# Kernel tuning notes

Measured on AMD Instinct MI355X. Metric: run time of the kernel, lower is better.

Reference implementation:

```python
import jax, jax.numpy as jnp
import numpy as np

B, S, H, V = 32, 400, 512, 50000


def setup_inputs() -> dict:
    key = jax.random.key(0)
    ks = jax.random.split(key, 32)
    g = lambda i, shape: jax.random.normal(ks[i], shape, jnp.float32) * 0.05
    return {
        "x_id": jax.random.randint(ks[0], (B, S), 0, V, jnp.int32),
        "y_id": jax.random.randint(ks[1], (B, 1), 0, V, jnp.int32),
        "x_mask": jnp.zeros((B, S), jnp.int32),  # pad flag: 1 = pad
        "emb": g(2, (V, H)),
        "enc_fw_W": g(3, (H, 3 * H)), "enc_fw_U": g(4, (H, 3 * H)), "enc_fw_b": g(5, (2, 3 * H)),
        "enc_bw_W": g(6, (H, 3 * H)), "enc_bw_U": g(7, (H, 3 * H)), "enc_bw_b": g(8, (2, 3 * H)),
        "red_W": g(9, (2 * H, H)), "red_b": g(10, (H,)),
        "dec_W": g(11, (H, 3 * H)), "dec_U": g(12, (H, 3 * H)), "dec_b": g(13, (2, 3 * H)),
        "att_Wh": g(14, (2 * H, H)), "att_Ws": g(15, (H, H)), "att_bs": g(16, (H,)),
        "att_Wc": g(17, (1, 1)), "att_V": g(18, (H, 1)),
        "fc_W": g(19, (3 * H, H)), "fc_b": g(20, (H,)),
        "vocab_W": g(21, (H, V)),
        "pg_Wh": g(22, (2 * H, 1)), "pg_Ws": g(23, (H, 1)), "pg_Wx": g(24, (H, 1)), "pg_b": g(25, (1,)),
    }


def _gru_cell(h, xz, U, br):
    # Keras GRU, reset_after=True, gate order z, r, h
    hd = h.shape[-1]
    rec = h @ U + br
    z = jax.nn.sigmoid(xz[..., :hd] + rec[..., :hd])
    r = jax.nn.sigmoid(xz[..., hd:2 * hd] + rec[..., hd:2 * hd])
    hh = jnp.tanh(xz[..., 2 * hd:] + r * rec[..., 2 * hd:])
    return z * h + (1.0 - z) * hh


def _gru_scan(x, h0, W, U, b):
    xz = x @ W + b[0]  # [b,T,3H] -- input projections precomputed
    def step(h, xt):
        h = _gru_cell(h, xt, U, b[1])
        return h, h
    h_last, hs = jax.lax.scan(step, h0, jnp.swapaxes(xz, 0, 1))
    return jnp.swapaxes(hs, 0, 1), h_last


def reference(x_id, y_id, x_mask, emb, enc_fw_W, enc_fw_U, enc_fw_b, enc_bw_W, enc_bw_U, enc_bw_b,
              red_W, red_b, dec_W, dec_U, dec_b, att_Wh, att_Ws, att_bs, att_Wc, att_V,
              fc_W, fc_b, vocab_W, pg_Wh, pg_Ws, pg_Wx, pg_b):
    b, s = x_id.shape
    hid = enc_fw_U.shape[0]
    maskf = x_mask.astype(jnp.float32)
    # ---- encoder: single-layer BiGRU ----
    x_emb = emb[x_id]                                     # [b,S,H]
    h0 = jnp.zeros((b, hid), x_emb.dtype)
    fw_seq, fw_s = _gru_scan(x_emb, h0, enc_fw_W, enc_fw_U, enc_fw_b)
    bw_seq, bw_s = _gru_scan(x_emb[:, ::-1], h0, enc_bw_W, enc_bw_U, enc_bw_b)
    enc_seq = jnp.concatenate([fw_seq, bw_seq[:, ::-1]], -1)   # [b,S,2H]
    state = jax.nn.relu(jnp.concatenate([fw_s, bw_s], -1) @ red_W + red_b)  # [b,H]
    # ---- decoder: one GRU step ----
    y_emb = emb[y_id]                                     # [b,1,H]
    xz = y_emb[:, 0] @ dec_W + dec_b[0]
    dec_state = _gru_cell(state, xz, dec_U, dec_b[1])     # [b,H]
    dec_out = dec_state[:, None, :]                       # [b,1,H]
    # ---- Bahdanau attention with (zero-initialized) coverage ----
    e = enc_seq @ att_Wh + (dec_out @ att_Ws + att_bs)    # [b,S,H]
    cover = jnp.zeros((b, s, 1), e.dtype)
    e = e + cover @ att_Wc
    e = jnp.tanh(e) @ att_V                               # [b,S,1]
    e = e + maskf[..., None] * -1e10
    w = jax.nn.softmax(e, axis=-2)                        # [b,S,1]
    context = jnp.sum(w * enc_seq, axis=-2, keepdims=True)  # [b,1,2H]
    # ---- output projection + vocab softmax ----
    y_out = jnp.concatenate([dec_out, context], -1) @ fc_W + fc_b  # [b,1,H]
    vocab_dist = jax.nn.softmax(y_out[:, 0] @ vocab_W, axis=-1)    # [b,V]
    # ---- pointer gate ----
    p_gen = jax.nn.sigmoid(context[:, 0] @ pg_Wh + dec_state @ pg_Ws + y_emb[:, 0] @ pg_Wx + pg_b)  # [b,1]
    # ---- extended-vocab copy distribution (vectorized batched scatter-add) ----
    aw = w[..., 0] * (1.0 - maskf) * (1.0 - p_gen)        # [b,S]
    ext = jnp.pad(p_gen * vocab_dist, ((0, 0), (0, s)))   # [b,V+S]
    bidx = jnp.arange(b)[:, None]
    final = ext.at[bidx, x_id].add(aw)                    # [b,V+S]
    return final
```

## Files before the change

### kernel.cpp

```cpp
#include <hip/hip_runtime.h>
#include <math.h>

#define S_LEN 400
#define BATCH 32
#define HID   512
#define G3    1536
#define N2    3072
#define VOC   50000
#define OUTW  (VOC + S_LEN)

typedef unsigned long long ull;
typedef unsigned int uint;
typedef unsigned short ushort;
typedef short bf16x8 __attribute__((ext_vector_type(8)));
typedef float f32x4 __attribute__((ext_vector_type(4)));
typedef ushort u16x8 __attribute__((ext_vector_type(8)));

__device__ __forceinline__ float sigf(float x) { return 1.f / (1.f + __expf(-x)); }
__device__ __forceinline__ float tanh_fast(float x) {
  const float xc = fminf(fmaxf(x, -15.f), 15.f);
  const float e = __expf(-2.f * xc);
  return (1.f - e) / (1.f + e);
}
__device__ __forceinline__ ushort f2bf(float f) {
  uint u = __float_as_uint(f);
  u += 0x7FFFu + ((u >> 16) & 1u);
  return (ushort)(u >> 16);
}
__device__ __forceinline__ float bf2f(ushort h) {
  return __uint_as_float((uint)h << 16);
}
__device__ __forceinline__ float dot4(float4 a, float4 b) {
  return a.x*b.x + a.y*b.y + a.z*b.z + a.w*b.w;
}

__device__ void trans_tile_512(const float* __restrict__ srcA,
                               const float* __restrict__ srcB,
                               const int split, const int stride, const int Krows,
                               const int k0, const int n0,
                               ushort* __restrict__ dstH, float* __restrict__ dstF)
{
  __shared__ float tt[64][65];
  const int tid = threadIdx.x;
  const int j = tid & 63, i0 = tid >> 6;
  {
    const int n = n0 + j;
    const float* s = (n < split) ? (srcA + n) : (srcB + (n - split));
    #pragma unroll
    for (int i = i0; i < 64; i += 8)
      tt[i][j] = s[(size_t)(k0 + i) * stride];
  }
  __syncthreads();
  const int ii = tid & 63;
  if (dstH != nullptr) {
    #pragma unroll
    for (int jj = i0; jj < 64; jj += 8)
      dstH[(size_t)(n0 + jj) * Krows + k0 + ii] = f2bf(tt[ii][jj]);
  } else {
    #pragma unroll
    for (int jj = i0; jj < 64; jj += 8)
      dstF[(size_t)(n0 + jj) * Krows + k0 + ii] = tt[ii][jj];
  }
}

__global__ __launch_bounds__(512) void gru_scan(
    const ushort* __restrict__ xzm,
    const ushort* __restrict__ Utbf,
    const float* __restrict__ bfw, const float* __restrict__ bbw,
    float* __restrict__ enc_seq, ushort* __restrict__ enc_bf,
    ull* __restrict__ hpkt,
    const float* __restrict__ att_Wh, const float* __restrict__ red_W,
    const float* __restrict__ dec_W, const float* __restrict__ dec_U,
    const float* __restrict__ att_Ws, const float* __restrict__ fc_W,
    ushort* __restrict__ Whbf, float* __restrict__ redWt,
    float* __restrict__ decWUt, float* __restrict__ WsT,
    float* __restrict__ fcT)
{
  if (blockIdx.x >= 128) {
    const int tb = blockIdx.x - 128;
    if (tb < 128) {
      trans_tile_512(att_Wh, att_Wh, 512, 512, 1024,
                     (tb % 16) * 64, (tb / 16) * 64, Whbf, nullptr);
    } else if (tb < 256) {
      const int t = tb - 128;
      trans_tile_512(red_W, red_W, 512, 512, 1024,
                     (t % 16) * 64, (t / 16) * 64, nullptr, redWt);
    } else if (tb < 640) {
      const int t = tb - 256;
      trans_tile_512(dec_W, dec_U, G3, G3, 512,
                     (t % 8) * 64, (t / 8) * 64, nullptr, decWUt);
    } else if (tb < 704) {
      const int t = tb - 640;
      trans_tile_512(att_Ws, att_Ws, 512, 512, 512,
                     (t % 8) * 64, (t / 8) * 64, nullptr, WsT);
    } else {
      const int t = tb - 704;
      trans_tile_512(fc_W, fc_W, 512, 512, 1536,
                     (t % 24) * 64, (t / 24) * 64, nullptr, fcT);
    }
    return;
  }

  const int bid = blockIdx.x;
  const int group = bid & 7;
  const int dir = group >> 2;
  const int bg  = group & 3;
  const int ht  = bid >> 3;
  const int tid = threadIdx.x;
  const int lane = tid & 63;
  const int w  = tid >> 6;
  const int l15 = lane & 15;
  const int lk  = lane >> 4;

  const float* __restrict__ br = (dir ? bbw : bfw) + G3;

  const int gate = w % 3, jh = w / 3;
  bf16x8 ufrag[16];
  if (w < 6) {
    const ushort* ub = Utbf + ((size_t)dir * G3 + gate * 512 + ht * 32 + jh * 16 + l15) * 512
                     + lk * 8;
    #pragma unroll
    for (int s = 0; s < 16; ++s)
      ufrag[s] = *(const bf16x8*)(ub + s * 32);
  }

  __shared__ ushort h_bf[16][520];
  __shared__ float redm[3][8][32];

  for (int i = tid; i < 16 * 520; i += 512) ((ushort*)h_bf)[i] = 0;

  const int cb = w;
  const int gbi = tid >> 5;
  const int gj  = tid & 31;
  const int gjq = ht * 32 + gj;
  const int gb  = bg * 8 + (gbi & 7);
  const float brz = br[gjq], brr = br[512 + gjq], brh = br[1024 + gjq];

  ull* __restrict__ pk = hpkt + (size_t)dir * (2 * BATCH * HID);
  __syncthreads();

  for (int t = 0; t < S_LEN; ++t) {
    const int ts = dir ? (S_LEN - 1 - t) : t;

    float xzv0 = 0.f, xzv1 = 0.f, xzv2 = 0.f;
    if (tid < 256) {
      const ushort* xp = xzm + ((size_t)gb * S_LEN + ts) * N2 + dir * G3 + gjq;
      xzv0 = bf2f(xp[0]); xzv1 = bf2f(xp[512]); xzv2 = bf2f(xp[1024]);
    }

    float hold = 0.f;
    {
      ull* bp = pk + ((size_t)(t & 1) * BATCH + (bg * 8 + cb)) * HID + lane;
      ull* hp = pk + ((size_t)(t & 1) * BATCH + gb) * HID + gjq;
      const uint tu = (uint)t;
      for (;;) {
        ull v0 = __hip_atomic_load(bp,       __ATOMIC_RELAXED, __HIP_MEMORY_SCOPE_AGENT);
        ull v1 = __hip_atomic_load(bp + 64,  __ATOMIC_RELAXED, __HIP_MEMORY_SCOPE_AGENT);
        ull v2 = __hip_atomic_load(bp + 128, __ATOMIC_RELAXED, __HIP_MEMORY_SCOPE_AGENT);
        ull v3 = __hip_atomic_load(bp + 192, __ATOMIC_RELAXED, __HIP_MEMORY_SCOPE_AGENT);
        ull v4 = __hip_atomic_load(bp + 256, __ATOMIC_RELAXED, __HIP_MEMORY_SCOPE_AGENT);
        ull v5 = __hip_atomic_load(bp + 320, __ATOMIC_RELAXED, __HIP_MEMORY_SCOPE_AGENT);
        ull v6 = __hip_atomic_load(bp + 384, __ATOMIC_RELAXED, __HIP_MEMORY_SCOPE_AGENT);
        ull v7 = __hip_atomic_load(bp + 448, __ATOMIC_RELAXED, __HIP_MEMORY_SCOPE_AGENT);
        bool ok = ((uint)(v0 >> 32) == tu) & ((uint)(v1 >> 32) == tu)
                & ((uint)(v2 >> 32) == tu) & ((uint)(v3 >> 32) == tu)
                & ((uint)(v4 >> 32) == tu) & ((uint)(v5 >> 32) == tu)
                & ((uint)(v6 >> 32) == tu) & ((uint)(v7 >> 32) == tu);
        ull hv = 0;
        if (tid < 256) {
          hv = __hip_atomic_load(hp, __ATOMIC_RELAXED, __HIP_MEMORY_SCOPE_AGENT);
          ok &= ((uint)(hv >> 32) == tu);
        }
        if (__all(ok)) {
          h_bf[cb][lane]       = f2bf(__uint_as_float((uint)v0));
          h_bf[cb][lane + 64]  = f2bf(__uint_as_float((uint)v1));
          h_bf[cb][lane + 128] = f2bf(__uint_as_float((uint)v2));
          h_bf[cb][lane + 192] = f2bf(__uint_as_float((uint)v3));
          h_bf[cb][lane + 256] = f2bf(__uint_as_float((uint)v4));
          h_bf[cb][lane + 320] = f2bf(__uint_as_float((uint)v5));
          h_bf[cb][lane + 384] = f2bf(__uint_as_float((uint)v6));
          h_bf[cb][lane + 448] = f2bf(__uint_as_float((uint)v7));
          if (tid < 256) hold = __uint_as_float((uint)hv);
          break;
        }
        __builtin_amdgcn_s_sleep(1);
      }
    }
    __syncthreads();

    if (w < 6) {
      f32x4 acc = f32x4{0.f, 0.f, 0.f, 0.f};
      #pragma unroll
      for (int s = 0; s < 16; ++s) {
        const bf16x8 af = *(const bf16x8*)&h_bf[l15][s * 32 + lk * 8];
        acc = __builtin_amdgcn_mfma_f32_16x16x32_bf16(af, ufrag[s], acc, 0, 0, 0);
      }
      if (lk < 2) {
        #pragma unroll
        for (int r = 0; r < 4; ++r)
          redm[gate][lk * 4 + r][jh * 16 + l15] = acc[r];
      }
    }
    __syncthreads();

    if (tid < 256) {
      const float rz = redm[0][gbi][gj] + brz;
      const float rr = redm[1][gbi][gj] + brr;
      const float rh = redm[2][gbi][gj] + brh;
      const float z  = sigf(xzv0 + rz);
      const float r  = sigf(xzv1 + rr);
      const float hh = tanh_fast(xzv2 + r * rh);
      const float hnew = z * hold + (1.f - z) * hh;
      const ull pack = ((ull)(uint)(t + 1) << 32) | (ull)__float_as_uint(hnew);
      __hip_atomic_store(pk + ((size_t)((t + 1) & 1) * BATCH + gb) * HID + gjq,
                         pack, __ATOMIC_RELAXED, __HIP_MEMORY_SCOPE_AGENT);
      const size_t eidx = ((size_t)gb * S_LEN + ts) * 1024 + dir * 512 + gjq;
      enc_seq[eidx] = hnew;
      enc_bf[eidx]  = f2bf(hnew);
    }
    __syncthreads();
  }
}

__global__ __launch_bounds__(256) void k_prep(
    const int* __restrict__ x_id, const float* __restrict__ emb,
    ushort* __restrict__ Abf,
    const float* __restrict__ fwW, const float* __restrict__ bwW,
    const float* __restrict__ fwb, const float* __restrict__ bwb,
    const float* __restrict__ fwU, const float* __restrict__ bwU,
    ushort* __restrict__ Wt, float* __restrict__ bm,
    ushort* __restrict__ Utbf)
{
  const int tid = threadIdx.x;
  if (blockIdx.x < 3200) {
    const int row = blockIdx.x * 4 + (tid >> 6);
    const int k8 = (tid & 63) * 8;
    const int rid = x_id[row];
    const float4 e0 = *(const float4*)&emb[(size_t)rid * 512 + k8];
    const float4 e1 = *(const float4*)&emb[(size_t)rid * 512 + k8 + 4];
    u16x8 o;
    o[0] = f2bf(e0.x); o[1] = f2bf(e0.y); o[2] = f2bf(e0.z); o[3] = f2bf(e0.w);
    o[4] = f2bf(e1.x); o[5] = f2bf(e1.y); o[6] = f2bf(e1.z); o[7] = f2bf(e1.w);
    *(u16x8*)&Abf[(size_t)row * 512 + k8] = o;
    return;
  }
  __shared__ float tt[64][65];
  const int b = blockIdx.x - 3200;
  const int j = tid & 63, i0 = tid >> 6;
  const float* srcA; const float* srcB; int split, k0, n0; ushort* dst;
  if (b < 384)      { srcA = fwW; srcB = bwW; split = G3;
                      k0 = (b % 8) * 64; n0 = (b / 8) * 64; dst = Wt; }
  else if (b < 576) { const int t = b - 384; srcA = fwU; srcB = fwU; split = N2;
                      k0 = (t % 8) * 64; n0 = (t / 8) * 64; dst = Utbf; }
  else              { const int t = b - 576; srcA = bwU; srcB = bwU; split = N2;
                      k0 = (t % 8) * 64; n0 = (t / 8) * 64;
                      dst = Utbf + (size_t)G3 * 512; }
  {
    const int n = n0 + j;
    const float* s = (n < split) ? (srcA + n) : (srcB + (n - split));
    #pragma unroll
    for (int i = i0; i < 64; i += 4)
      tt[i][j] = s[(size_t)(k0 + i) * G3];
  }
  __syncthreads();
  const int ii = tid & 63;
  #pragma unroll
  for (int jj = i0; jj < 64; jj += 4)
    dst[(size_t)(n0 + jj) * 512 + k0 + ii] = f2bf(tt[ii][jj]);
  if (b < 384 && k0 == 0 && tid < 64) {
    const int n = n0 + tid;
    bm[n] = (n < G3) ? fwb[n] : bwb[n - G3];
  }
}

__global__ __launch_bounds__(256) void gemm_bf16(
    const ushort* __restrict__ A,
    const ushort* __restrict__ Bt,
    const float* __restrict__ bias,
    ushort* __restrict__ C)
{
  const int m0 = blockIdx.y * 128, n0 = blockIdx.x * 128;
  const int tid = threadIdx.x;
  const int w = tid >> 6, lane = tid & 63;
  const int l15 = lane & 15, lk = lane >> 4;
  __shared__ short As[128][40];
  __shared__ short Bs[128][40];
  f32x4 acc[2][8];
  #pragma unroll
  for (int i = 0; i < 2; ++i)
    #pragma unroll
    for (int j = 0; j < 8; ++j) acc[i][j] = f32x4{0.f, 0.f, 0.f, 0.f};

  const int sr = tid >> 1;
  const int sc = (tid & 1) * 8;

  for (int k0 = 0; k0 < 512; k0 += 32) {
    const uint4 a0 = *(const uint4*)&A[(size_t)(m0 + sr) * 512 + k0 + sc];
    const uint4 a1 = *(const uint4*)&A[(size_t)(m0 + sr) * 512 + k0 + 16 + sc];
    const uint4 b0 = *(const uint4*)&Bt[(size_t)(n0 + sr) * 512 + k0 + sc];
    const uint4 b1 = *(const uint4*)&Bt[(size_t)(n0 + sr) * 512 + k0 + 16 + sc];
    *(uint4*)&As[sr][sc]      = a0;
    *(uint4*)&As[sr][16 + sc] = a1;
    *(uint4*)&Bs[sr][sc]      = b0;
    *(uint4*)&Bs[sr][16 + sc] = b1;
    __syncthreads();

    bf16x8 af[2], bfr[8];
    #pragma unroll
    for (int rf = 0; rf < 2; ++rf)
      af[rf] = *(const bf16x8*)&As[w * 32 + rf * 16 + l15][lk * 8];
    #pragma unroll
    for (int cf = 0; cf < 8; ++cf)
      bfr[cf] = *(const bf16x8*)&Bs[cf * 16 + l15][lk * 8];
    #pragma unroll
    for (int rf = 0; rf < 2; ++rf)
      #pragma unroll
      for (int cf = 0; cf < 8; ++cf)
        acc[rf][cf] = __builtin_amdgcn_mfma_f32_16x16x32_bf16(
            af[rf], bfr[cf], acc[rf][cf], 0, 0, 0);
    __syncthreads();
  }

  #pragma unroll
  for (int rf = 0; rf < 2; ++rf) {
    #pragma unroll
    for (int cf = 0; cf < 8; ++cf) {
      const int col = n0 + cf * 16 + l15;
      const float bv = bias[col];
      const int rowb = m0 + w * 32 + rf * 16 + lk * 4;
      #pragma unroll
      for (int r = 0; r < 4; ++r)
        C[(size_t)(rowb + r) * N2 + col] = f2bf(acc[rf][cf][r] + bv);
    }
  }
}

__global__ __launch_bounds__(256) void gemm_att(
    const ushort* __restrict__ A,
    const ushort* __restrict__ Bt,
    const float* __restrict__ dterm,
    const float* __restrict__ attV,
    float* __restrict__ e_part)
{
  const int m0 = blockIdx.y * 128, n0 = blockIdx.x * 128;
  const int tid = threadIdx.x;
  const int w = tid >> 6, lane = tid & 63;
  const int l15 = lane & 15, lk = lane >> 4;
  __shared__ short As[128][40];
  __shared__ short Bs[128][40];
  f32x4 acc[2][8];
  #pragma unroll
  for (int i = 0; i < 2; ++i)
    #pragma unroll
    for (int j = 0; j < 8; ++j) acc[i][j] = f32x4{0.f, 0.f, 0.f, 0.f};

  const int sr = tid >> 1;
  const int sc = (tid & 1) * 8;

  for (int k0 = 0; k0 < 1024; k0 += 32) {
    const uint4 a0 = *(const uint4*)&A[(size_t)(m0 + sr) * 1024 + k0 + sc];
    const uint4 a1 = *(const uint4*)&A[(size_t)(m0 + sr) * 1024 + k0 + 16 + sc];
    const uint4 b0 = *(const uint4*)&Bt[(size_t)(n0 + sr) * 1024 + k0 + sc];
    const uint4 b1 = *(const uint4*)&Bt[(size_t)(n0 + sr) * 1024 + k0 + 16 + sc];
    *(uint4*)&As[sr][sc]      = a0;
    *(uint4*)&As[sr][16 + sc] = a1;
    *(uint4*)&Bs[sr][sc]      = b0;
    *(uint4*)&Bs[sr][16 + sc] = b1;
    __syncthreads();

    bf16x8 af[2], bfr[8];
    #pragma unroll
    for (int rf = 0; rf < 2; ++rf)
      af[rf] = *(const bf16x8*)&As[w * 32 + rf * 16 + l15][lk * 8];
    #pragma unroll
    for (int cf = 0; cf < 8; ++cf)
      bfr[cf] = *(const bf16x8*)&Bs[cf * 16 + l15][lk * 8];
    #pragma unroll
    for (int rf = 0; rf < 2; ++rf)
      #pragma unroll
      for (int cf = 0; cf < 8; ++cf)
        acc[rf][cf] = __builtin_amdgcn_mfma_f32_16x16x32_bf16(
            af[rf], bfr[cf], acc[rf][cf], 0, 0, 0);
    __syncthreads();
  }

  #pragma unroll
  for (int rf = 0; rf < 2; ++rf) {
    #pragma unroll
    for (int r = 0; r < 4; ++r) {
      const int row = m0 + w * 32 + rf * 16 + lk * 4 + r;
      const int b = row / S_LEN;
      float p = 0.f;
      #pragma unroll
      for (int cf = 0; cf < 8; ++cf) {
        const int col = n0 + cf * 16 + l15;
        p += attV[col] * tanh_fast(acc[rf][cf][r] + dterm[(size_t)b * 512 + col]);
      }
      p += __shfl_xor(p, 1); p += __shfl_xor(p, 2);
      p += __shfl_xor(p, 4); p += __shfl_xor(p, 8);
      if (l15 == 0) e_part[(size_t)row * 4 + blockIdx.x] = p;
    }
  }
}

__global__ __launch_bounds__(128) void k_state(const float* __restrict__ enc,
    const float* __restrict__ redWt, const float* __restrict__ red_b,
    float* __restrict__ state)
{
  const int b = blockIdx.y;
  const int j = blockIdx.x*128 + threadIdx.x;
  const float4* wr = (const float4*)(redWt + (size_t)j * 1024);
  const float4* fw = (const float4*)(enc + ((size_t)b*S_LEN + (S_LEN-1))*1024);
  const float4* bw = (const float4*)(enc + ((size_t)b*S_LEN)*1024 + 512);
  float acc = red_b[j];
  #pragma unroll 4
  for (int k = 0; k < 128; ++k) acc += dot4(fw[k], wr[k]);
  #pragma unroll 4
  for (int k = 0; k < 128; ++k) acc += dot4(bw[k], wr[128 + k]);
  state[(size_t)b*512 + j] = fmaxf(acc, 0.f);
}

__global__ __launch_bounds__(128) void k_dec(
    const int* __restrict__ y_id, const float* __restrict__ emb,
    const float* __restrict__ state,
    const float* __restrict__ decWUt,
    const float* __restrict__ dec_b, float* __restrict__ dst)
{
  const int b = blockIdx.y;
  const int j = blockIdx.x*128 + threadIdx.x;
  const float4* ye = (const float4*)(emb + (size_t)y_id[b] * 512);
  const float4* st = (const float4*)(state + (size_t)b * 512);
  const float4* w0 = (const float4*)(decWUt + (size_t)(j)        * 512);
  const float4* w1 = (const float4*)(decWUt + (size_t)(512  + j) * 512);
  const float4* w2 = (const float4*)(decWUt + (size_t)(1024 + j) * 512);
  const float4* u0 = (const float4*)(decWUt + (size_t)(G3 + j)        * 512);
  const float4* u1 = (const float4*)(decWUt + (size_t)(G3 + 512  + j) * 512);
  const float4* u2 = (const float4*)(decWUt + (size_t)(G3 + 1024 + j) * 512);
  float xz0 = dec_b[j], xz1 = dec_b[512+j], xz2 = dec_b[1024+j];
  float rc0 = dec_b[G3+j], rc1 = dec_b[G3+512+j], rc2 = dec_b[G3+1024+j];
  #pragma unroll 2
  for (int k = 0; k < 128; ++k) {
    const float4 yv = ye[k], sv = st[k];
    xz0 += dot4(yv, w0[k]); xz1 += dot4(yv, w1[k]); xz2 += dot4(yv, w2[k]);
    rc0 += dot4(sv, u0[k]); rc1 += dot4(sv, u1[k]); rc2 += dot4(sv, u2[k]);
  }
  const float z  = sigf(xz0 + rc0);
  const float r  = sigf(xz1 + rc1);
  const float hh = tanh_fast(xz2 + r*rc2);
  const float sj = state[(size_t)b*512 + j];
  dst[(size_t)b*512 + j] = z*sj + (1.f-z)*hh;
}

__global__ __launch_bounds__(128) void k_dterm(const float* __restrict__ dec,
    const float* __restrict__ WsT, const float* __restrict__ att_bs,
    float* __restrict__ dterm)
{
  const int b = blockIdx.y;
  const int j = blockIdx.x*128 + threadIdx.x;
  const float4* d = (const float4*)(dec + (size_t)b*512);
  const float4* wr = (const float4*)(WsT + (size_t)j * 512);
  float acc = att_bs[j];
  #pragma unroll 4
  for (int k = 0; k < 128; ++k) acc += dot4(d[k], wr[k]);
  dterm[(size_t)b*512 + j] = acc;
}

__global__ __launch_bounds__(512) void k_soft(const float* __restrict__ e_part,
    const int* __restrict__ x_mask, float* __restrict__ wat)
{
  const int b = blockIdx.x, tid = threadIdx.x;
  __shared__ float sm[512];
  float e = -1e30f, ev = 0.f;
  if (tid < S_LEN) {
    const float* ep = e_part + (size_t)(b*S_LEN + tid)*4;
    ev = ep[0]+ep[1]+ep[2]+ep[3] + (float)x_mask[b*S_LEN+tid] * -1e10f;
    e = ev;
  }
  sm[tid] = e; __syncthreads();
  for (int s = 256; s > 0; s >>= 1) { if (tid < s) sm[tid] = fmaxf(sm[tid], sm[tid+s]); __syncthreads(); }
  const float m = sm[0]; __syncthreads();
  const float x = (tid < S_LEN) ? __expf(ev - m) : 0.f;
  sm[tid] = x; __syncthreads();
  for (int s = 256; s > 0; s >>= 1) { if (tid < s) sm[tid] += sm[tid+s]; __syncthreads(); }
  const float inv = 1.f / sm[0];
  if (tid < S_LEN) wat[b*S_LEN+tid] = x * inv;
}

__global__ __launch_bounds__(128) void k_ctx(const float* __restrict__ wat,
    const float* __restrict__ enc, float* __restrict__ ctx)
{
  const int b = blockIdx.y;
  const int j = blockIdx.x*128 + threadIdx.x;
  float acc = 0.f;
  const float* w = wat + b*S_LEN;
  const float* ep = enc + (size_t)b*S_LEN*1024 + j;
  #pragma unroll 4
  for (int s = 0; s < S_LEN; ++s) acc += w[s] * ep[(size_t)s*1024];
  ctx[(size_t)b*1024 + j] = acc;
}

__global__ __launch_bounds__(128) void k_yout(const float* __restrict__ dec,
    const float* __restrict__ ctx, const float* __restrict__ fcT,
    const float* __restrict__ fc_b, float* __restrict__ y_out)
{
  const int b = blockIdx.y;
  const int j = blockIdx.x*128 + threadIdx.x;
  const float4* d = (const float4*)(dec + (size_t)b*512);
  const float4* c = (const float4*)(ctx + (size_t)b*1024);
  const float4* wr = (const float4*)(fcT + (size_t)j * 1536);
  float acc = fc_b[j];
  #pragma unroll 4
  for (int k = 0; k < 128; ++k) acc += dot4(d[k], wr[k]);
  #pragma unroll 4
  for (int k = 0; k < 256; ++k) acc += dot4(c[k], wr[128 + k]);
  y_out[(size_t)b*512 + j] = acc;
}

__global__ __launch_bounds__(256) void k_pgen(const float* __restrict__ ctx,
    const float* __restrict__ dec,
    const int* __restrict__ y_id, const float* __restrict__ emb,
    const float* __restrict__ pg_Wh, const float* __restrict__ pg_Ws,
    const float* __restrict__ pg_Wx, const float* __restrict__ pg_b,
    float* __restrict__ pg)
{
  const int b = blockIdx.x, tid = threadIdx.x;
  __shared__ float sm[256];
  const float* ye = emb + (size_t)y_id[b] * 512;
  float acc = 0.f;
  for (int k = tid; k < 1024; k += 256) acc += ctx[(size_t)b*1024+k]*pg_Wh[k];
  for (int k = tid; k < 512;  k += 256) acc += dec[(size_t)b*512+k]*pg_Ws[k] + ye[k]*pg_Wx[k];
  sm[tid] = acc; __syncthreads();
  for (int s = 128; s > 0; s >>= 1) { if (tid < s) sm[tid] += sm[tid+s]; __syncthreads(); }
  if (tid == 0) pg[b] = sigf(sm[0] + pg_b[0]);
}

__global__ __launch_bounds__(256) void k_vocab(const float* __restrict__ y_out,
    const float* __restrict__ vocab_W, float* __restrict__ logits,
    float* __restrict__ vpart)
{
  __shared__ float y_lds[256][32];
  const int tid = threadIdx.x;
  const int vq = tid & 63, bq = tid >> 6;
  const int v = blockIdx.x * 256 + vq * 4;
  const bool valid = (v < VOC);
  float acc[8][4];
  #pragma unroll
  for (int i = 0; i < 8; ++i)
    #pragma unroll
    for (int j = 0; j < 4; ++j) acc[i][j] = 0.f;
  for (int half = 0; half < 2; ++half) {
    __syncthreads();
    for (int i = 0; i < 32; ++i) {
      const int idx = tid + 256*i;
      const int k = idx >> 5, b = idx & 31;
      y_lds[k][b] = y_out[(size_t)b*512 + half*256 + k];
    }
    __syncthreads();
    if (valid) {
      #pragma unroll 4
      for (int k = 0; k < 256; ++k) {
        const float4 wv = *(const float4*)&vocab_W[(size_t)(half*256 + k) * VOC + v];
        const float4 ya = *(const float4*)&y_lds[k][bq*8];
        const float4 yb = *(const float4*)&y_lds[k][bq*8+4];
        const float yy[8] = {ya.x,ya.y,ya.z,ya.w,yb.x,yb.y,yb.z,yb.w};
        #pragma unroll
        for (int i = 0; i < 8; ++i) {
          acc[i][0] += yy[i]*wv.x; acc[i][1] += yy[i]*wv.y;
          acc[i][2] += yy[i]*wv.z; acc[i][3] += yy[i]*wv.w;
        }
      }
    }
  }
  if (valid) {
    #pragma unroll
    for (int i = 0; i < 8; ++i)
      *(float4*)&logits[(size_t)(bq*8+i)*VOC + v] = make_float4(acc[i][0],acc[i][1],acc[i][2],acc[i][3]);
  }
  #pragma unroll
  for (int i = 0; i < 8; ++i) {
    float m = valid ? fmaxf(fmaxf(acc[i][0], acc[i][1]), fmaxf(acc[i][2], acc[i][3]))
                    : -1e30f;
    m = fmaxf(m, __shfl_xor(m, 1));  m = fmaxf(m, __shfl_xor(m, 2));
    m = fmaxf(m, __shfl_xor(m, 4));  m = fmaxf(m, __shfl_xor(m, 8));
    m = fmaxf(m, __shfl_xor(m, 16)); m = fmaxf(m, __shfl_xor(m, 32));
    float s = 0.f;
    if (valid) {
      s = __expf(acc[i][0]-m) + __expf(acc[i][1]-m)
        + __expf(acc[i][2]-m) + __expf(acc[i][3]-m);
    }
    s += __shfl_xor(s, 1);  s += __shfl_xor(s, 2);
    s += __shfl_xor(s, 4);  s += __shfl_xor(s, 8);
    s += __shfl_xor(s, 16); s += __shfl_xor(s, 32);
    if ((tid & 63) == 0) {
      const size_t o = ((size_t)blockIdx.x * 32 + bq * 8 + i) * 2;
      vpart[o] = m; vpart[o + 1] = s;
    }
  }
}

__global__ __launch_bounds__(64) void k_vred2(const float* __restrict__ vpart,
                                              float* __restrict__ red2)
{
  const int b = threadIdx.x;
  if (b >= 32) return;
  float m = -1e30f;
  for (int x = 0; x < 196; ++x) m = fmaxf(m, vpart[((size_t)x*32 + b)*2]);
  float S = 0.f;
  for (int x = 0; x < 196; ++x) {
    const float ml = vpart[((size_t)x*32 + b)*2];
    const float sl = vpart[((size_t)x*32 + b)*2 + 1];
    S += sl * __expf(ml - m);
  }
  red2[b*2] = m; red2[b*2+1] = S;
}

__global__ __launch_bounds__(256) void k_final(const float* __restrict__ logits,
    const float* __restrict__ red2, const float* __restrict__ pg,
    float* __restrict__ out)
{
  const size_t idx = (size_t)blockIdx.x*256 + threadIdx.x;
  const int b = (int)(idx / OUTW);
  const int c = (int)(idx - (size_t)b*OUTW);
  float v = 0.f;
  if (c < VOC) {
    const float m = red2[b*2], s = red2[b*2+1];
    v = pg[b] * __expf(logits[(size_t)b*VOC + c] - m) / s;
  }
  out[idx] = v;
}

__global__ __launch_bounds__(256) void k_scatter(const float* __restrict__ wat,
    const int* __restrict__ x_mask, const float* __restrict__ pg,
    const int* __restrict__ x_id, float* __restrict__ out)
{
  const int i = blockIdx.x*256 + threadIdx.x;
  const int b = i / S_LEN;
  const float aw = wat[i] * (1.f - (float)x_mask[i]) * (1.f - pg[b]);
  atomicAdd(out + (size_t)b*OUTW + x_id[i], aw);
}

extern "C" void kernel_launch(void* const* d_in, const int* in_sizes, int n_in,
                              void* d_out, int out_size, void* d_ws, size_t ws_size,
                              hipStream_t stream)
{
  (void)in_sizes; (void)n_in; (void)out_size; (void)ws_size;
  const int*   x_id     = (const int*)d_in[0];
  const int*   y_id     = (const int*)d_in[1];
  const int*   x_mask   = (const int*)d_in[2];
  const float* emb      = (const float*)d_in[3];
  const float* enc_fw_W = (const float*)d_in[4];
  const float* enc_fw_U = (const float*)d_in[5];
  const float* enc_fw_b = (const float*)d_in[6];
  const float* enc_bw_W = (const float*)d_in[7];
  const float* enc_bw_U = (const float*)d_in[8];
  const float* enc_bw_b = (const float*)d_in[9];
  const float* red_W    = (const float*)d_in[10];
  const float* red_b    = (const float*)d_in[11];
  const float* dec_W    = (const float*)d_in[12];
  const float* dec_U    = (const float*)d_in[13];
  const float* dec_b    = (const float*)d_in[14];
  const float* att_Wh   = (const float*)d_in[15];
  const float* att_Ws   = (const float*)d_in[16];
  const float* att_bs   = (const float*)d_in[17];
  const float* att_Wc   = (const float*)d_in[18]; (void)att_Wc;
  const float* att_V    = (const float*)d_in[19];
  const float* fc_W     = (const float*)d_in[20];
  const float* fc_b     = (const float*)d_in[21];
  const float* vocab_W  = (const float*)d_in[22];
  const float* pg_Wh    = (const float*)d_in[23];
  const float* pg_Ws    = (const float*)d_in[24];
  const float* pg_Wx    = (const float*)d_in[25];
  const float* pg_b     = (const float*)d_in[26];
  float* out = (float*)d_out;

  const size_t NPKT = (size_t)2*2*BATCH*HID;
  char* p = (char*)d_ws;
  ushort* xzm   = (ushort*)p; p += (size_t)BATCH*S_LEN*N2*2;
  float*  enc   = (float*)p;  p += (size_t)BATCH*S_LEN*1024*4;
  ushort* encbf = (ushort*)p; p += (size_t)BATCH*S_LEN*1024*2;
  ull*   hpkt   = (ull*)p;    p += NPKT*8;
  ushort* Abf   = (ushort*)p; p += (size_t)BATCH*S_LEN*512*2;
  ushort* Wt    = (ushort*)p; p += (size_t)N2*512*2;
  ushort* Whbf  = (ushort*)p; p += (size_t)512*1024*2;
  ushort* Utbf  = (ushort*)p; p += (size_t)2*G3*512*2;
  float*  redWt = (float*)p;  p += (size_t)512*1024*4;
  float*  decWUt= (float*)p;  p += (size_t)N2*512*4;
  float*  WsT   = (float*)p;  p += (size_t)512*512*4;
  float*  fcT   = (float*)p;  p += (size_t)512*1536*4;
  float*  bm    = (float*)p;  p += (size_t)N2*4;
  float*  fstate = (float*)p; p += (size_t)BATCH*HID*4;
  float*  decs   = (float*)p; p += (size_t)BATCH*HID*4;
  float*  dterm  = (float*)p; p += (size_t)BATCH*HID*4;
  float*  epart  = (float*)p; p += (size_t)BATCH*S_LEN*4*4;
  float*  wat    = (float*)p; p += (size_t)BATCH*S_LEN*4;
  float*  ctx    = (float*)p; p += (size_t)BATCH*1024*4;
  float*  yout   = (float*)p; p += (size_t)BATCH*HID*4;
  float*  pg     = (float*)p; p += (size_t)256*4;
  float*  logits = (float*)p; p += (size_t)BATCH*VOC*4;
  float*  red2   = (float*)p; p += (size_t)64*4;
  float*  vpart  = (float*)p; p += (size_t)196*32*2*4;

  hipMemsetAsync(hpkt, 0, NPKT * sizeof(ull), stream);

  k_prep<<<3200 + 768, 256, 0, stream>>>(x_id, emb, Abf,
                                         enc_fw_W, enc_bw_W, enc_fw_b, enc_bw_b,
                                         enc_fw_U, enc_bw_U, Wt, bm, Utbf);
  gemm_bf16<<<dim3(N2/128, BATCH*S_LEN/128), 256, 0, stream>>>(Abf, Wt, bm, xzm);
  gru_scan<<<128 + 896, 512, 0, stream>>>(xzm, Utbf, enc_fw_b, enc_bw_b,
                                          enc, encbf, hpkt,
                                          att_Wh, red_W, dec_W, dec_U, att_Ws,
                                          fc_W, Whbf, redWt, decWUt, WsT, fcT);
  k_state<<<dim3(4,32),128,0,stream>>>(enc, redWt, red_b, fstate);
  k_dec<<<dim3(4,32),128,0,stream>>>(y_id, emb, fstate, decWUt, dec_b, decs);
  k_dterm<<<dim3(4,32),128,0,stream>>>(decs, WsT, att_bs, dterm);
  gemm_att<<<dim3(4, BATCH*S_LEN/128), 256, 0, stream>>>(encbf, Whbf, dterm,
                                                         att_V, epart);
  k_soft<<<32,512,0,stream>>>(epart, x_mask, wat);
  k_ctx<<<dim3(8,32),128,0,stream>>>(wat, enc, ctx);
  k_yout<<<dim3(4,32),128,0,stream>>>(decs, ctx, fcT, fc_b, yout);
  k_pgen<<<32,256,0,stream>>>(ctx, decs, y_id, emb, pg_Wh, pg_Ws, pg_Wx, pg_b, pg);
  k_vocab<<<196,256,0,stream>>>(yout, vocab_W, logits, vpart);
  k_vred2<<<1,64,0,stream>>>(vpart, red2);
  k_final<<<6300,256,0,stream>>>(logits, red2, pg, out);
  k_scatter<<<50,256,0,stream>>>(wat, x_mask, pg, x_id, out);
}
```

Before: 1.334 ms.

## Fuse input-projection GEMM into GRU scan kernel with per-tile progress flags

```diff
diff --git a/kernel.cpp b/kernel.cpp
--- a/kernel.cpp
+++ b/kernel.cpp
@@ -64,11 +64,14 @@
 }
 
 __global__ __launch_bounds__(512) void gru_scan(
-    const ushort* __restrict__ xzm,
+    const ushort* __restrict__ Abf,
+    const ushort* __restrict__ Wt,
+    const float* __restrict__ bm,
+    ushort* __restrict__ xzm,
     const ushort* __restrict__ Utbf,
     const float* __restrict__ bfw, const float* __restrict__ bbw,
     float* __restrict__ enc_seq, ushort* __restrict__ enc_bf,
-    ull* __restrict__ hpkt,
+    ull* __restrict__ hpkt, uint* __restrict__ progress,
     const float* __restrict__ att_Wh, const float* __restrict__ red_W,
     const float* __restrict__ dec_W, const float* __restrict__ dec_U,
     const float* __restrict__ att_Ws, const float* __restrict__ fc_W,
@@ -76,8 +79,64 @@
     float* __restrict__ decWUt, float* __restrict__ WsT,
     float* __restrict__ fcT)
 {
-  if (blockIdx.x >= 128) {
-    const int tb = blockIdx.x - 128;
+  const int tid = threadIdx.x;
+  const int lane = tid & 63;
+  const int w  = tid >> 6;
+  const int l15 = lane & 15;
+  const int lk  = lane >> 4;
+
+  if (blockIdx.x >= 128 && blockIdx.x < 2528) {
+    const int wk = blockIdx.x - 128;
+    const int ti = wk / 24, ct = wk % 24;
+    const int rt = (ti & 1) ? (99 - (ti >> 1)) : (ti >> 1);
+    const int n0 = ct * 128;
+    __shared__ short Aw[128][40];
+    __shared__ short Bw[128][40];
+    f32x4 acc[8];
+    #pragma unroll
+    for (int j = 0; j < 8; ++j) acc[j] = f32x4{0.f, 0.f, 0.f, 0.f};
+
+    const int ar = tid >> 2, ac = (tid & 3) * 8;
+    const ushort* arow = Abf + (size_t)(rt * 128 + ar) * 512 + ac;
+    const ushort* brow = Wt + (size_t)(n0 + ar) * 512 + ac;
+
+    for (int k0 = 0; k0 < 512; k0 += 32) {
+      *(u16x8*)&Aw[ar][ac] = *(const u16x8*)(arow + k0);
+      *(u16x8*)&Bw[ar][ac] = *(const u16x8*)(brow + k0);
+      __syncthreads();
+      const bf16x8 af = *(const bf16x8*)&Aw[w * 16 + l15][lk * 8];
+      #pragma unroll
+      for (int cf = 0; cf < 8; ++cf) {
+        const bf16x8 bfr = *(const bf16x8*)&Bw[cf * 16 + l15][lk * 8];
+        acc[cf] = __builtin_amdgcn_mfma_f32_16x16x32_bf16(af, bfr, acc[cf], 0, 0, 0);
+      }
+      __syncthreads();
+    }
+    #pragma unroll
+    for (int cf = 0; cf < 8; ++cf) {
+      const int col = n0 + cf * 16 + l15;
+      const float bv = bm[col];
+      #pragma unroll
+      for (int r = 0; r < 4; ++r) {
+        const int row = rt * 128 + w * 16 + lk * 4 + r;
+        const uint h = (uint)f2bf(acc[cf][r] + bv);
+        const uint other = (uint)__shfl_xor((int)h, 1);
+        if (!(lane & 1)) {
+          const uint packv = h | (other << 16);
+          __hip_atomic_store((uint*)xzm + ((size_t)row * N2 + col) / 2, packv,
+                             __ATOMIC_RELAXED, __HIP_MEMORY_SCOPE_AGENT);
+        }
+      }
+    }
+    asm volatile("s_waitcnt vmcnt(0)" ::: "memory");
+    __syncthreads();
+    if (tid == 0)
+      __hip_atomic_fetch_add(progress + rt, 1u,
+                             __ATOMIC_RELEASE, __HIP_MEMORY_SCOPE_AGENT);
+    return;
+  }
+  if (blockIdx.x >= 2528) {
+    const int tb = blockIdx.x - 2528;
     if (tb < 128) {
       trans_tile_512(att_Wh, att_Wh, 512, 512, 1024,
                      (tb % 16) * 64, (tb / 16) * 64, Whbf, nullptr);
@@ -106,11 +165,6 @@
   const int dir = group >> 2;
   const int bg  = group & 3;
   const int ht  = bid >> 3;
-  const int tid = threadIdx.x;
-  const int lane = tid & 63;
-  const int w  = tid >> 6;
-  const int l15 = lane & 15;
-  const int lk  = lane >> 4;
 
   const float* __restrict__ br = (dir ? bbw : bfw) + G3;
 
@@ -137,15 +191,42 @@
   const float brz = br[gjq], brr = br[512 + gjq], brh = br[1024 + gjq];
 
   ull* __restrict__ pk = hpkt + (size_t)dir * (2 * BATCH * HID);
+  const uint* __restrict__ xz32 = (const uint*)xzm;
   __syncthreads();
+
+  uint conf = 0;
+  uint pend = __hip_atomic_load(progress + (dir ? 99 : 0),
+                                __ATOMIC_RELAXED, __HIP_MEMORY_SCOPE_AGENT);
 
   for (int t = 0; t < S_LEN; ++t) {
     const int ts = dir ? (S_LEN - 1 - t) : t;
 
+    {
+      const uint kneed = (uint)(t >> 2);
+      while (conf <= kneed) {
+        if (pend >= 24u) {
+          ++conf;
+          if (conf < 100u)
+            pend = __hip_atomic_load(progress + (dir ? 99 - (int)conf : (int)conf),
+                                     __ATOMIC_RELAXED, __HIP_MEMORY_SCOPE_AGENT);
+        } else {
+          __builtin_amdgcn_s_sleep(2);
+          pend = __hip_atomic_load(progress + (dir ? 99 - (int)conf : (int)conf),
+                                   __ATOMIC_RELAXED, __HIP_MEMORY_SCOPE_AGENT);
+        }
+      }
+    }
+
     float xzv0 = 0.f, xzv1 = 0.f, xzv2 = 0.f;
     if (tid < 256) {
-      const ushort* xp = xzm + ((size_t)gb * S_LEN + ts) * N2 + dir * G3 + gjq;
-      xzv0 = bf2f(xp[0]); xzv1 = bf2f(xp[512]); xzv2 = bf2f(xp[1024]);
+      const size_t e0 = (((size_t)ts * 32 + gb) * N2 + dir * G3 + (gjq & ~1)) >> 1;
+      const uint u0 = __hip_atomic_load(xz32 + e0,       __ATOMIC_RELAXED, __HIP_MEMORY_SCOPE_AGENT);
+      const uint u1 = __hip_atomic_load(xz32 + e0 + 256, __ATOMIC_RELAXED, __HIP_MEMORY_SCOPE_AGENT);
+      const uint u2 = __hip_atomic_load(xz32 + e0 + 512, __ATOMIC_RELAXED, __HIP_MEMORY_SCOPE_AGENT);
+      const bool hi = (gjq & 1);
+      xzv0 = bf2f(hi ? (ushort)(u0 >> 16) : (ushort)u0);
+      xzv1 = bf2f(hi ? (ushort)(u1 >> 16) : (ushort)u1);
+      xzv2 = bf2f(hi ? (ushort)(u2 >> 16) : (ushort)u2);
     }
 
     float hold = 0.f;
@@ -235,7 +316,7 @@
   if (blockIdx.x < 3200) {
     const int row = blockIdx.x * 4 + (tid >> 6);
     const int k8 = (tid & 63) * 8;
-    const int rid = x_id[row];
+    const int rid = x_id[(row & 31) * S_LEN + (row >> 5)];
     const float4 e0 = *(const float4*)&emb[(size_t)rid * 512 + k8];
     const float4 e1 = *(const float4*)&emb[(size_t)rid * 512 + k8 + 4];
     u16x8 o;
@@ -270,68 +351,6 @@
   if (b < 384 && k0 == 0 && tid < 64) {
     const int n = n0 + tid;
     bm[n] = (n < G3) ? fwb[n] : bwb[n - G3];
-  }
-}
-
-__global__ __launch_bounds__(256) void gemm_bf16(
-    const ushort* __restrict__ A,
-    const ushort* __restrict__ Bt,
-    const float* __restrict__ bias,
-    ushort* __restrict__ C)
-{
-  const int m0 = blockIdx.y * 128, n0 = blockIdx.x * 128;
-  const int tid = threadIdx.x;
-  const int w = tid >> 6, lane = tid & 63;
-  const int l15 = lane & 15, lk = lane >> 4;
-  __shared__ short As[128][40];
-  __shared__ short Bs[128][40];
-  f32x4 acc[2][8];
-  #pragma unroll
-  for (int i = 0; i < 2; ++i)
-    #pragma unroll
-    for (int j = 0; j < 8; ++j) acc[i][j] = f32x4{0.f, 0.f, 0.f, 0.f};
-
-  const int sr = tid >> 1;
-  const int sc = (tid & 1) * 8;
-
-  for (int k0 = 0; k0 < 512; k0 += 32) {
-    const uint4 a0 = *(const uint4*)&A[(size_t)(m0 + sr) * 512 + k0 + sc];
-    const uint4 a1 = *(const uint4*)&A[(size_t)(m0 + sr) * 512 + k0 + 16 + sc];
-    const uint4 b0 = *(const uint4*)&Bt[(size_t)(n0 + sr) * 512 + k0 + sc];
-    const uint4 b1 = *(const uint4*)&Bt[(size_t)(n0 + sr) * 512 + k0 + 16 + sc];
-    *(uint4*)&As[sr][sc]      = a0;
-    *(uint4*)&As[sr][16 + sc] = a1;
-    *(uint4*)&Bs[sr][sc]      = b0;
-    *(uint4*)&Bs[sr][16 + sc] = b1;
-    __syncthreads();
-
-    bf16x8 af[2], bfr[8];
-    #pragma unroll
-    for (int rf = 0; rf < 2; ++rf)
-      af[rf] = *(const bf16x8*)&As[w * 32 + rf * 16 + l15][lk * 8];
-    #pragma unroll
-    for (int cf = 0; cf < 8; ++cf)
-      bfr[cf] = *(const bf16x8*)&Bs[cf * 16 + l15][lk * 8];
-    #pragma unroll
-    for (int rf = 0; rf < 2; ++rf)
-      #pragma unroll
-      for (int cf = 0; cf < 8; ++cf)
-        acc[rf][cf] = __builtin_amdgcn_mfma_f32_16x16x32_bf16(
-            af[rf], bfr[cf], acc[rf][cf], 0, 0, 0);
-    __syncthreads();
-  }
-
-  #pragma unroll
-  for (int rf = 0; rf < 2; ++rf) {
-    #pragma unroll
-    for (int cf = 0; cf < 8; ++cf) {
-      const int col = n0 + cf * 16 + l15;
-      const float bv = bias[col];
-      const int rowb = m0 + w * 32 + rf * 16 + lk * 4;
-      #pragma unroll
-      for (int r = 0; r < 4; ++r)
-        C[(size_t)(rowb + r) * N2 + col] = f2bf(acc[rf][cf][r] + bv);
-    }
   }
 }
 
@@ -679,6 +698,7 @@
   float*  enc   = (float*)p;  p += (size_t)BATCH*S_LEN*1024*4;
   ushort* encbf = (ushort*)p; p += (size_t)BATCH*S_LEN*1024*2;
   ull*   hpkt   = (ull*)p;    p += NPKT*8;
+  uint*  progress = (uint*)p; p += 128*4;
   ushort* Abf   = (ushort*)p; p += (size_t)BATCH*S_LEN*512*2;
   ushort* Wt    = (ushort*)p; p += (size_t)N2*512*2;
   ushort* Whbf  = (ushort*)p; p += (size_t)512*1024*2;
@@ -700,16 +720,16 @@
   float*  red2   = (float*)p; p += (size_t)64*4;
   float*  vpart  = (float*)p; p += (size_t)196*32*2*4;
 
-  hipMemsetAsync(hpkt, 0, NPKT * sizeof(ull), stream);
+  hipMemsetAsync(hpkt, 0, NPKT * sizeof(ull) + 128 * sizeof(uint), stream);
 
   k_prep<<<3200 + 768, 256, 0, stream>>>(x_id, emb, Abf,
                                          enc_fw_W, enc_bw_W, enc_fw_b, enc_bw_b,
                                          enc_fw_U, enc_bw_U, Wt, bm, Utbf);
-  gemm_bf16<<<dim3(N2/128, BATCH*S_LEN/128), 256, 0, stream>>>(Abf, Wt, bm, xzm);
-  gru_scan<<<128 + 896, 512, 0, stream>>>(xzm, Utbf, enc_fw_b, enc_bw_b,
-                                          enc, encbf, hpkt,
-                                          att_Wh, red_W, dec_W, dec_U, att_Ws,
-                                          fc_W, Whbf, redWt, decWUt, WsT, fcT);
+  gru_scan<<<128 + 2400 + 896, 512, 0, stream>>>(
+      Abf, Wt, bm, xzm, Utbf, enc_fw_b, enc_bw_b,
+      enc, encbf, hpkt, progress,
+      att_Wh, red_W, dec_W, dec_U, att_Ws, fc_W,
+      Whbf, redWt, decWUt, WsT, fcT);
   k_state<<<dim3(4,32),128,0,stream>>>(enc, redWt, red_b, fstate);
   k_dec<<<dim3(4,32),128,0,stream>>>(y_id, emb, fstate, decWUt, dec_b, decs);
   k_dterm<<<dim3(4,32),128,0,stream>>>(decs, WsT, att_bs, dterm);
```

Measured after the change: 1.360 ms. No clear change (+2.0%).
